# Performance work log

Hardware: AMD Instinct MI355X
Metric: run time of the kernel (lower is better)

The kernel has to match this reference:

```python
import jax, jax.numpy as jnp
import numpy as np

# Constructor constants (from init_kwargs)
B, F, K, D = 4096, 2048, 64, 8
VOL_TEMP = 0.5   # SoftVolume temperature -> softplus beta = 1/VOL_TEMP
INT_TEMP = 0.1   # GumbelIntersection temperature
EPS = 1e-23      # box_embeddings soft-volume clamp


def setup_inputs() -> dict:
    key = jax.random.key(0)
    ks = jax.random.split(key, 9)
    def lin(k, shp, fan_in):
        return (jax.random.normal(k, shp, jnp.float32) / np.sqrt(fan_in)).astype(jnp.float32)
    return {
        "features": jax.random.normal(ks[0], (B, F), jnp.float32),
        # stacked per-concept projectors: Linear(F -> 2D) for each of K concepts
        "Wp": lin(ks[1], (K, F, 2 * D), F),
        "bp": lin(ks[2], (K, 2 * D), F),
        # stacked per-concept prob predictors: Linear(2D -> 1)
        "Wprob": lin(ks[3], (K, 2 * D), 2 * D),
        "bprob": lin(ks[4], (K,), 2 * D),
        # classifier heads
        "Wbox": lin(ks[5], (K * 2 * D, 1), K * 2 * D),
        "bbox": lin(ks[6], (1,), K * 2 * D),
        "Wrel": lin(ks[7], (K * K, 1), K * K),
        "brel": lin(ks[8], (1,), K * K),
    }


def _log_soft_volume(z, Z):
    # box_embeddings SoftVolume: sum_d log(max(softplus(Z - z, beta=1/vol_temp), eps))
    beta = 1.0 / VOL_TEMP
    side = jax.nn.softplus(beta * (Z - z)) / beta
    return jnp.sum(jnp.log(jnp.maximum(side, EPS)), axis=-1)


def reference(features, Wp, bp, Wprob, bprob, Wbox, bbox, Wrel, brel):
    b = features.shape[0]
    # all K projectors as one batched GEMM: [B,F] x [K,F,2D] -> [B,K,2D]
    theta = jnp.einsum('bf,kfd->bkd', features, Wp) + bp
    theta = theta.reshape(b, K, 2, D)
    # MinDeltaBoxTensor: z = theta[...,0,:], Z = z + softplus(theta[...,1,:])
    z = theta[:, :, 0, :]                       # [B,K,D]
    Z = z + jax.nn.softplus(theta[:, :, 1, :])  # [B,K,D]

    coords = jnp.concatenate([z, Z], axis=-1)   # [B,K,2D]
    logits = jnp.einsum('bkd,kd->bk', coords, Wprob) + bprob
    concept_probs = jax.nn.sigmoid(logits)      # [B,K]

    # Pairwise Gumbel intersection over all (i,j) concept pairs (vectorized k^2 loop)
    t = INT_TEMP
    zi, zj = z[:, :, None, :], z[:, None, :, :]   # [B,K,1,D] vs [B,1,K,D]
    Zi, Zj = Z[:, :, None, :], Z[:, None, :, :]
    z_int = t * jnp.logaddexp(zi / t, zj / t)
    z_int = jnp.maximum(z_int, jnp.maximum(zi, zj))
    Z_int = -t * jnp.logaddexp(-Zi / t, -Zj / t)
    Z_int = jnp.minimum(Z_int, jnp.minimum(Zi, Zj))

    lv_int = _log_soft_volume(z_int, Z_int)       # [B,K,K]
    lv_box = _log_soft_volume(z, Z)               # [B,K]
    # P(i|j) = vol(i ^ j) / vol(j)
    cond = jnp.clip(jnp.exp(lv_int - lv_box[:, None, :]), 1e-6, 1.0 - 1e-6)  # [B,K,K]

    # scale each box's coords by its concept prob, flatten as [z_i, Z_i] per concept
    p = concept_probs[:, :, None]
    flat_boxes = jnp.concatenate([z * p, Z * p], axis=-1).reshape(b, K * 2 * D)
    flat_rel = cond.reshape(b, K * K)

    final_logit = flat_boxes @ Wbox + bbox + flat_rel @ Wrel + brel  # [B,1]
    task_probs = jax.nn.sigmoid(final_logit)
    return task_probs, concept_probs, cond
```

## Files before the change

kernel.cpp:

```cpp
#include <hip/hip_runtime.h>
#include <cstdint>
#include <cstddef>


typedef __bf16 bf16_t;
typedef __bf16 bf16x4 __attribute__((ext_vector_type(4)));
typedef __bf16 bf16x8 __attribute__((ext_vector_type(8)));
typedef float floatx4 __attribute__((ext_vector_type(4)));

#define LOG2E 1.4426950408889634f
#define LN2 0.6931471805599453f
#define K1C 14.426950408889634f
#define K3C 2.8853900817779268f

__device__ __forceinline__ float ex2(float x) { return __builtin_exp2f(x); }
__device__ __forceinline__ float lg2(float x) { return __builtin_log2f(x); }

__device__ __forceinline__ void gload16(const bf16_t* g, bf16_t* l) {
  __builtin_amdgcn_global_load_lds(
      (const __attribute__((address_space(1))) void*)g,
      (__attribute__((address_space(3))) void*)l, 16, 0, 0);
}

__global__ __launch_bounds__(256) void prep_a(const float* __restrict__ A,
                                              bf16_t* __restrict__ Ah,
                                              bf16_t* __restrict__ Al) {
  const size_t i = ((size_t)blockIdx.x * 256 + threadIdx.x) * 8;
  const float4 v0 = *reinterpret_cast<const float4*>(A + i);
  const float4 v1 = *reinterpret_cast<const float4*>(A + i + 4);
  const float x[8] = {v0.x, v0.y, v0.z, v0.w, v1.x, v1.y, v1.z, v1.w};
  bf16x8 h, l;
#pragma unroll
  for (int u = 0; u < 8; ++u) {
    const __bf16 hv = (__bf16)x[u];
    h[u] = hv;
    l[u] = (__bf16)(x[u] - (float)hv);
  }
  *reinterpret_cast<bf16x8*>(Ah + i) = h;
  *reinterpret_cast<bf16x8*>(Al + i) = l;
}

__global__ __launch_bounds__(256, 2) void prep_b(const float* __restrict__ Wp,
                                                 bf16_t* __restrict__ Bt) {
  __shared__ float tile[128][17];
  const int kc = blockIdx.x;
  const int f0 = blockIdx.y * 128;
  const int t = threadIdx.x;
  {
    const int fl = t >> 1, dh = (t & 1) * 8;
    const float* g = Wp + ((size_t)kc * 2048 + f0 + fl) * 16 + dh;
    float4 v0 = *reinterpret_cast<const float4*>(g);
    float4 v1 = *reinterpret_cast<const float4*>(g + 4);
    tile[fl][dh + 0] = v0.x; tile[fl][dh + 1] = v0.y;
    tile[fl][dh + 2] = v0.z; tile[fl][dh + 3] = v0.w;
    tile[fl][dh + 4] = v1.x; tile[fl][dh + 5] = v1.y;
    tile[fl][dh + 6] = v1.z; tile[fl][dh + 7] = v1.w;
  }
  __syncthreads();
  {
    const int d = t >> 4, fi = (t & 15) * 8;
    float x[8];
#pragma unroll
    for (int u = 0; u < 8; ++u) x[u] = tile[fi + u][d];
    bf16x8 hv, lv;
#pragma unroll
    for (int u = 0; u < 8; ++u) {
      __bf16 h = (__bf16)x[u];
      hv[u] = h;
      lv[u] = (__bf16)(x[u] - (float)h);
    }
    const size_t row = (size_t)(kc * 16 + d) * 4096;
    *reinterpret_cast<bf16x8*>(Bt + row + f0 + fi) = hv;
    *reinterpret_cast<bf16x8*>(Bt + row + 2048 + f0 + fi) = lv;
  }
}

__global__ __launch_bounds__(256, 1) void gemm_theta(
    const bf16_t* __restrict__ Ahg, const bf16_t* __restrict__ Alg,
    const bf16_t* __restrict__ Bt, const float* __restrict__ bias,
    float* __restrict__ C) {
  __shared__ bf16_t lds[2][4][128 * 32];
  const int t = threadIdx.x;
  const int m0 = blockIdx.x * 128, n0 = blockIdx.y * 128;
  const int wave = t >> 6, lane = t & 63, quad = lane >> 4, l16 = lane & 15;
  const int wm = (wave >> 1) * 64, wn = (wave & 1) * 64;
  floatx4 acc[4][4] = {};

  const int srow = t >> 2;
  const int skey = (srow >> 1) & 3;
  const int c8 = (((t & 3) ^ skey)) * 8;
  const bf16_t* gAh0 = Ahg + (size_t)(m0 + srow) * 2048 + c8;
  const bf16_t* gAh1 = Ahg + (size_t)(m0 + 64 + srow) * 2048 + c8;
  const bf16_t* gAl0 = Alg + (size_t)(m0 + srow) * 2048 + c8;
  const bf16_t* gAl1 = Alg + (size_t)(m0 + 64 + srow) * 2048 + c8;
  const bf16_t* gBh0 = Bt + (size_t)(n0 + srow) * 4096 + c8;
  const bf16_t* gBh1 = Bt + (size_t)(n0 + 64 + srow) * 4096 + c8;

  auto stage = [&](int bf, int kk) {
    const int ko = kk * 32;
    gload16(gAh0 + ko, &lds[bf][0][t * 8]);
    gload16(gAh1 + ko, &lds[bf][0][(256 + t) * 8]);
    gload16(gAl0 + ko, &lds[bf][1][t * 8]);
    gload16(gAl1 + ko, &lds[bf][1][(256 + t) * 8]);
    gload16(gBh0 + ko, &lds[bf][2][t * 8]);
    gload16(gBh1 + ko, &lds[bf][2][(256 + t) * 8]);
    gload16(gBh0 + 2048 + ko, &lds[bf][3][t * 8]);
    gload16(gBh1 + 2048 + ko, &lds[bf][3][(256 + t) * 8]);
  };

  stage(0, 0);
  __syncthreads();

  const int fkey = (l16 >> 1) & 3;
  const int qa = (quad ^ fkey) * 8;

  int buf = 0;
  for (int kk = 0; kk < 64; ++kk) {
    if (kk < 63) stage(buf ^ 1, kk + 1);
    bf16x8 ah[4], al[4], bh[4], bl[4];
#pragma unroll
    for (int r = 0; r < 4; ++r) {
      const int off = (wm + r * 16 + l16) * 32 + qa;
      ah[r] = *reinterpret_cast<const bf16x8*>(&lds[buf][0][off]);
      al[r] = *reinterpret_cast<const bf16x8*>(&lds[buf][1][off]);
    }
#pragma unroll
    for (int c = 0; c < 4; ++c) {
      const int off = (wn + c * 16 + l16) * 32 + qa;
      bh[c] = *reinterpret_cast<const bf16x8*>(&lds[buf][2][off]);
      bl[c] = *reinterpret_cast<const bf16x8*>(&lds[buf][3][off]);
    }
#pragma unroll
    for (int r = 0; r < 4; ++r)
#pragma unroll
      for (int c = 0; c < 4; ++c) {
        acc[r][c] = __builtin_amdgcn_mfma_f32_16x16x32_bf16(ah[r], bh[c],
                                                            acc[r][c], 0, 0, 0);
        acc[r][c] = __builtin_amdgcn_mfma_f32_16x16x32_bf16(al[r], bh[c],
                                                            acc[r][c], 0, 0, 0);
        acc[r][c] = __builtin_amdgcn_mfma_f32_16x16x32_bf16(ah[r], bl[c],
                                                            acc[r][c], 0, 0, 0);
      }
    __syncthreads();
    buf ^= 1;
  }

#pragma unroll
  for (int r = 0; r < 4; ++r) {
    const int row0 = m0 + wm + r * 16 + quad * 4;
#pragma unroll
    for (int c = 0; c < 4; ++c) {
      const int col = n0 + wn + c * 16 + l16;
      const float bb = bias[col];
#pragma unroll
      for (int i = 0; i < 4; ++i)
        C[(size_t)(row0 + i) * 1024 + col] = acc[r][c][i] + bb;
    }
  }
}

__global__ __launch_bounds__(256, 2) void fused_pair(
    const float* __restrict__ Th, const float* __restrict__ Wprob,
    const float* __restrict__ bprob, const float* __restrict__ Wbox,
    const float* __restrict__ bbox, const float* __restrict__ Wrel,
    const float* __restrict__ brel, float* __restrict__ out) {
  __shared__ float sboxes[64][17];
  __shared__ float spinv[64];
  __shared__ float spc[64];
  __shared__ float swrel[4096];
  __shared__ float swbox[1024];
  __shared__ float sprod[2080];
  __shared__ float sred[4];

  const int b = blockIdx.x;
  const int t = threadIdx.x;
  const float* th = Th + (size_t)b * 1024;
  float* out_task = out;
  float* out_conc = out + 4096;
  float* out_cond = out + 266240;

  if (t < 64) {
    const int k = t;
    const float* thk = th + k * 16;
    float4 a0 = reinterpret_cast<const float4*>(thk)[0];
    float4 a1 = reinterpret_cast<const float4*>(thk)[1];
    float4 a2 = reinterpret_cast<const float4*>(thk)[2];
    float4 a3 = reinterpret_cast<const float4*>(thk)[3];
    float z[8] = {a0.x, a0.y, a0.z, a0.w, a1.x, a1.y, a1.z, a1.w};
    float w1[8] = {a2.x, a2.y, a2.z, a2.w, a3.x, a3.y, a3.z, a3.w};
    float dp = 1.0f;
    float logit = bprob[k];
#pragma unroll
    for (int d = 0; d < 8; ++d) {
      const float spv = LN2 * lg2(1.0f + ex2(w1[d] * LOG2E));
      const float Zd = z[d] + spv;
      const float denl = lg2(1.0f + ex2((Zd - z[d]) * K3C));
      dp *= denl;
      logit += z[d] * Wprob[k * 16 + d] + Zd * Wprob[k * 16 + 8 + d];
      sboxes[k][d] = z[d];
      sboxes[k][8 + d] = Zd;
    }
    spinv[k] = 1.0f / dp;
    const float pk = 1.0f / (1.0f + ex2(-logit * LOG2E));
    spc[k] = pk;
    out_conc[(size_t)b * 64 + k] = pk;
  }
#pragma unroll
  for (int q = 0; q < 4; ++q)
    reinterpret_cast<float4*>(swrel)[q * 256 + t] =
        reinterpret_cast<const float4*>(Wrel)[q * 256 + t];
  reinterpret_cast<float4*>(swbox)[t] = reinterpret_cast<const float4*>(Wbox)[t];
  __syncthreads();

#pragma unroll
  for (int q = 0; q < 9; ++q) {
    const int p = t + 256 * q;
    if (p < 2080) {
      int j = (int)((sqrtf((float)(8 * p + 1)) - 1.0f) * 0.5f);
      if ((j + 1) * (j + 2) / 2 <= p) ++j;
      if (j * (j + 1) / 2 > p) --j;
      const int i = p - j * (j + 1) / 2;
      float prodn = 1.0f;
#pragma unroll
      for (int d = 0; d < 8; ++d) {
        const float zi = sboxes[i][d], Zi = sboxes[i][8 + d];
        const float zjd = sboxes[j][d], Zjd = sboxes[j][8 + d];
        const float u = ex2(-fabsf(zi - zjd) * K1C);
        const float uZ = ex2(-fabsf(Zi - Zjd) * K1C);
        const float lsum = lg2(fmaf(u, uZ, 1.0f + u + uZ));
        const float gap = fminf(Zi, Zjd) - fmaxf(zi, zjd);
        const float E = ex2(fmaf(gap, K3C, -0.2f * lsum));
        prodn *= lg2(1.0f + E);
      }
      sprod[p] = prodn;
    }
  }
  __syncthreads();

  const int wv = t >> 6, lane = t & 63;
  const float pinvj = spinv[lane];
  float rsum = 0.0f;
#pragma unroll 4
  for (int ii = 0; ii < 16; ++ii) {
    const int i = wv * 16 + ii;
    const int lo = min(i, lane), hi = max(i, lane);
    const float prodn = sprod[hi * (hi + 1) / 2 + lo];
    float cond = prodn * pinvj;
    cond = fminf(fmaxf(cond, 1e-6f), 1.0f - 1e-6f);
    out_cond[(size_t)b * 4096 + i * 64 + lane] = cond;
    rsum = fmaf(cond, swrel[i * 64 + lane], rsum);
  }

  float bsum = 0.0f;
#pragma unroll
  for (int q = 0; q < 4; ++q) {
    const int idx = t + 256 * q;
    const int k = idx >> 4, c = idx & 15;
    bsum = fmaf(sboxes[k][c] * spc[k], swbox[idx], bsum);
  }
  float total = rsum + bsum;
#pragma unroll
  for (int off = 32; off > 0; off >>= 1) total += __shfl_down(total, off, 64);
  if (lane == 0) sred[wv] = total;
  __syncthreads();
  if (t == 0) {
    const float s = sred[0] + sred[1] + sred[2] + sred[3] + bbox[0] + brel[0];
    out_task[b] = 1.0f / (1.0f + ex2(-s * LOG2E));
  }
}

extern "C" void kernel_launch(void* const* d_in, const int* in_sizes, int n_in,
                              void* d_out, int out_size, void* d_ws, size_t ws_size,
                              hipStream_t stream) {
  const float* feat = (const float*)d_in[0];
  const float* Wp = (const float*)d_in[1];
  const float* bp = (const float*)d_in[2];
  const float* Wprob = (const float*)d_in[3];
  const float* bprob = (const float*)d_in[4];
  const float* Wbox = (const float*)d_in[5];
  const float* bbox = (const float*)d_in[6];
  const float* Wrel = (const float*)d_in[7];
  const float* brel = (const float*)d_in[8];
  float* out = (float*)d_out;

  char* ws = (char*)d_ws;
  bf16_t* Bt = (bf16_t*)ws;
  float* Th = (float*)(ws + (size_t)(8 << 20));
  bf16_t* Ah = (bf16_t*)(ws + (size_t)(24 << 20));
  bf16_t* Al = (bf16_t*)(ws + (size_t)(40 << 20));

  prep_a<<<4096, 256, 0, stream>>>(feat, Ah, Al);
  prep_b<<<dim3(64, 16), 256, 0, stream>>>(Wp, Bt);
  gemm_theta<<<dim3(32, 8), 256, 0, stream>>>(Ah, Al, Bt, bp, Th);
  fused_pair<<<4096, 256, 0, stream>>>(Th, Wprob, bprob, Wbox, bbox, Wrel, brel, out);
}
```

Baseline: 282.2 us.

## Index symmetric pairs by cyclic offset and remap GEMM block order

```diff
diff --git a/kernel.cpp b/kernel.cpp
--- a/kernel.cpp
+++ b/kernel.cpp
@@ -81,7 +81,9 @@
     float* __restrict__ C) {
   __shared__ bf16_t lds[2][4][128 * 32];
   const int t = threadIdx.x;
-  const int m0 = blockIdx.x * 128, n0 = blockIdx.y * 128;
+  const int bid = blockIdx.x;
+  const int m0 = (((bid & 7) << 2) + ((bid >> 3) & 3)) * 128;
+  const int n0 = (bid >> 5) * 128;
   const int wave = t >> 6, lane = t & 63, quad = lane >> 4, l16 = lane & 15;
   const int wm = (wave >> 1) * 64, wn = (wave & 1) * 64;
   floatx4 acc[4][4] = {};
@@ -169,7 +171,7 @@
   __shared__ float spc[64];
   __shared__ float swrel[4096];
   __shared__ float swbox[1024];
-  __shared__ float sprod[2080];
+  __shared__ float sprod[33 * 66];
   __shared__ float sred[4];
 
   const int b = blockIdx.x;
@@ -212,39 +214,59 @@
   reinterpret_cast<float4*>(swbox)[t] = reinterpret_cast<const float4*>(Wbox)[t];
   __syncthreads();
 
-#pragma unroll
-  for (int q = 0; q < 9; ++q) {
-    const int p = t + 256 * q;
-    if (p < 2080) {
-      int j = (int)((sqrtf((float)(8 * p + 1)) - 1.0f) * 0.5f);
-      if ((j + 1) * (j + 2) / 2 <= p) ++j;
-      if (j * (j + 1) / 2 > p) --j;
-      const int i = p - j * (j + 1) / 2;
-      float prodn = 1.0f;
-#pragma unroll
-      for (int d = 0; d < 8; ++d) {
-        const float zi = sboxes[i][d], Zi = sboxes[i][8 + d];
-        const float zjd = sboxes[j][d], Zjd = sboxes[j][8 + d];
-        const float u = ex2(-fabsf(zi - zjd) * K1C);
-        const float uZ = ex2(-fabsf(Zi - Zjd) * K1C);
-        const float lsum = lg2(fmaf(u, uZ, 1.0f + u + uZ));
-        const float gap = fminf(Zi, Zjd) - fmaxf(zi, zjd);
-        const float E = ex2(fmaf(gap, K3C, -0.2f * lsum));
-        prodn *= lg2(1.0f + E);
-      }
-      sprod[p] = prodn;
-    }
-  }
-  __syncthreads();
-
   const int wv = t >> 6, lane = t & 63;
+
+  float zi[8], Zi[8];
+#pragma unroll
+  for (int d = 0; d < 8; ++d) {
+    zi[d] = sboxes[lane][d];
+    Zi[d] = sboxes[lane][8 + d];
+  }
+
+#pragma unroll 2
+  for (int oo = 0; oo < 8; ++oo) {
+    const int o = wv * 8 + oo;
+    const int j = (lane + o) & 63;
+    float prodn = 1.0f;
+#pragma unroll
+    for (int d = 0; d < 8; ++d) {
+      const float zjd = sboxes[j][d], Zjd = sboxes[j][8 + d];
+      const float u = ex2(-fabsf(zi[d] - zjd) * K1C);
+      const float uZ = ex2(-fabsf(Zi[d] - Zjd) * K1C);
+      const float lsum = lg2(fmaf(u, uZ, 1.0f + u + uZ));
+      const float gap = fminf(Zi[d], Zjd) - fmaxf(zi[d], zjd);
+      const float E = ex2(fmaf(gap, K3C, -0.2f * lsum));
+      prodn *= lg2(1.0f + E);
+    }
+    sprod[o * 66 + lane] = prodn;
+  }
+  if (t < 64) {
+    const int j = (lane + 32) & 63;
+    float prodn = 1.0f;
+#pragma unroll
+    for (int d = 0; d < 8; ++d) {
+      const float zjd = sboxes[j][d], Zjd = sboxes[j][8 + d];
+      const float u = ex2(-fabsf(zi[d] - zjd) * K1C);
+      const float uZ = ex2(-fabsf(Zi[d] - Zjd) * K1C);
+      const float lsum = lg2(fmaf(u, uZ, 1.0f + u + uZ));
+      const float gap = fminf(Zi[d], Zjd) - fmaxf(zi[d], zjd);
+      const float E = ex2(fmaf(gap, K3C, -0.2f * lsum));
+      prodn *= lg2(1.0f + E);
+    }
+    sprod[32 * 66 + lane] = prodn;
+  }
+  __syncthreads();
+
   const float pinvj = spinv[lane];
   float rsum = 0.0f;
 #pragma unroll 4
   for (int ii = 0; ii < 16; ++ii) {
     const int i = wv * 16 + ii;
-    const int lo = min(i, lane), hi = max(i, lane);
-    const float prodn = sprod[hi * (hi + 1) / 2 + lo];
+    const int od = (lane - i) & 63;
+    const bool sel = od <= 32;
+    const int so = sel ? od : 64 - od;
+    const int si = sel ? i : lane;
+    const float prodn = sprod[so * 66 + si];
     float cond = prodn * pinvj;
     cond = fminf(fmaxf(cond, 1e-6f), 1.0f - 1e-6f);
     out_cond[(size_t)b * 4096 + i * 64 + lane] = cond;
@@ -291,6 +313,6 @@
 
   prep_a<<<4096, 256, 0, stream>>>(feat, Ah, Al);
   prep_b<<<dim3(64, 16), 256, 0, stream>>>(Wp, Bt);
-  gemm_theta<<<dim3(32, 8), 256, 0, stream>>>(Ah, Al, Bt, bp, Th);
+  gemm_theta<<<256, 256, 0, stream>>>(Ah, Al, Bt, bp, Th);
   fused_pair<<<4096, 256, 0, stream>>>(Th, Wprob, bprob, Wbox, bbox, Wrel, brel, out);
 }
```

Result: slower. 364.5 us (+29.2%).
